# Performance work log

Measured on AMD Instinct MI355X. Metric: run time of the kernel, lower is better.

The kernel has to match this reference:

```python
import jax, jax.numpy as jnp
import numpy as np

N_NODES = 50000
N_EDGES = 1600000
NUM_GRAPHS = 512
IN_FEATS = 128
HIDDEN = 128
NUM_CLASSES = 10
STEPS = 3


def setup_inputs() -> dict:
    key = jax.random.key(0)
    ks = jax.random.split(key, 16)
    x = jax.random.normal(ks[0], (N_NODES, IN_FEATS), dtype=jnp.float32)
    edge_index = jax.random.randint(ks[1], (2, N_EDGES), 0, N_NODES, dtype=jnp.int64)
    batch = jnp.sort(jax.random.randint(ks[2], (N_NODES,), 0, NUM_GRAPHS, dtype=jnp.int64))
    s = 0.1
    W1 = jax.random.normal(ks[3], (IN_FEATS, HIDDEN), dtype=jnp.float32) * s
    b1 = jnp.zeros((HIDDEN,), dtype=jnp.float32)
    W2 = jax.random.normal(ks[4], (HIDDEN, HIDDEN), dtype=jnp.float32) * s
    b2 = jnp.zeros((HIDDEN,), dtype=jnp.float32)
    # LSTM: input 2*HIDDEN -> hidden HIDDEN, torch gate order i,f,g,o
    Wih = jax.random.normal(ks[5], (4 * HIDDEN, 2 * HIDDEN), dtype=jnp.float32) * s
    Whh = jax.random.normal(ks[6], (4 * HIDDEN, HIDDEN), dtype=jnp.float32) * s
    bih = jnp.zeros((4 * HIDDEN,), dtype=jnp.float32)
    bhh = jnp.zeros((4 * HIDDEN,), dtype=jnp.float32)
    Wl1 = jax.random.normal(ks[7], (2 * HIDDEN, HIDDEN), dtype=jnp.float32) * s
    bl1 = jnp.zeros((HIDDEN,), dtype=jnp.float32)
    Wl2 = jax.random.normal(ks[8], (HIDDEN, NUM_CLASSES), dtype=jnp.float32) * s
    bl2 = jnp.zeros((NUM_CLASSES,), dtype=jnp.float32)
    return dict(x=x, edge_index=edge_index, batch=batch, W1=W1, b1=b1, W2=W2, b2=b2,
                Wih=Wih, Whh=Whh, bih=bih, bhh=bhh, Wl1=Wl1, bl1=bl1, Wl2=Wl2, bl2=bl2)


def gcn_conv(x, src, dst, W, b, n_nodes):
    # PyG GCNConv: add self-loops, sym-normalized scatter-add aggregation
    loop = jnp.arange(n_nodes, dtype=src.dtype)
    s = jnp.concatenate([src, loop])
    d = jnp.concatenate([dst, loop])
    deg = jax.ops.segment_sum(jnp.ones_like(d, dtype=x.dtype), d, num_segments=n_nodes)
    dinv = jnp.where(deg > 0, jax.lax.rsqrt(jnp.maximum(deg, 1.0)), 0.0)
    norm = dinv[s] * dinv[d]  # [E+N]
    h = x @ W  # [N, out]
    agg = jax.ops.segment_sum(norm[:, None] * h[s], d, num_segments=n_nodes)
    return agg + b


def segment_softmax(e, seg, num_segments):
    m = jax.ops.segment_max(e, seg, num_segments=num_segments)
    m = jnp.where(jnp.isfinite(m), m, 0.0)
    z = jnp.exp(e - m[seg])
    denom = jax.ops.segment_sum(z, seg, num_segments=num_segments)
    return z / denom[seg]


def set2set(x, batch, Wih, Whh, bih, bhh, num_graphs, steps):
    D = x.shape[1]
    h = jnp.zeros((num_graphs, D), dtype=x.dtype)
    c = jnp.zeros((num_graphs, D), dtype=x.dtype)
    q_star = jnp.zeros((num_graphs, 2 * D), dtype=x.dtype)
    for _ in range(steps):
        gates = q_star @ Wih.T + h @ Whh.T + bih + bhh  # [B, 4D]
        i, f, g, o = jnp.split(gates, 4, axis=-1)
        c = jax.nn.sigmoid(f) * c + jax.nn.sigmoid(i) * jnp.tanh(g)
        h = jax.nn.sigmoid(o) * jnp.tanh(c)
        q = h
        e = jnp.sum(x * q[batch], axis=-1)  # [N]
        a = segment_softmax(e, batch, num_graphs)
        r = jax.ops.segment_sum(a[:, None] * x, batch, num_segments=num_graphs)  # [B, D]
        q_star = jnp.concatenate([q, r], axis=-1)
    return q_star


def reference(x, edge_index, batch, W1, b1, W2, b2, Wih, Whh, bih, bhh, Wl1, bl1, Wl2, bl2):
    n = x.shape[0]
    src, dst = edge_index[0], edge_index[1]
    h = jax.nn.relu(gcn_conv(x, src, dst, W1, b1, n))
    h = jax.nn.relu(gcn_conv(h, src, dst, W2, b2, n))
    out = set2set(h, batch, Wih, Whh, bih, bhh, NUM_GRAPHS, STEPS)  # [B, 2D]
    out = jax.nn.relu(out @ Wl1 + bl1)
    return out @ Wl2 + bl2
```

## Files before the change

kernel.cpp:

```cpp
#include <hip/hip_runtime.h>
#include <hip/hip_bf16.h>
#include <math.h>

#define N_NODES 50000
#define N_EDGES 1600000
#define NUM_GRAPHS 512
#define HIDDEN 128
#define NUM_CLASSES 10
#define STEPS 3

#define NB_SHIFT 6
#define NODES_PER_B (1 << NB_SHIFT)
#define NBUK ((N_NODES + NODES_PER_B - 1) / NODES_PER_B)
#define EPB 8192
#define NBLK ((N_EDGES + EPB - 1) / EPB)
#define MAXR 144
#define NCH 7

__device__ inline float bf2f(unsigned short h) {
    union { unsigned int u; float f; } v; v.u = ((unsigned int)h) << 16; return v.f;
}
__device__ inline unsigned short f2bf(float f) {
    union { float f; unsigned int u; } v; v.f = f;
    unsigned int r = (v.u + 0x7FFFu + ((v.u >> 16) & 1u)) >> 16;
    return (unsigned short)r;
}


__global__ void k_detect(const int* p, int* flag, int npairs) {
    int i = blockIdx.x * blockDim.x + threadIdx.x;
    if (i < npairs) {
        int v = p[2 * i + 1];
        if (v != 0) atomicOr(flag, 1);
    }
}

__global__ void k_goff(const void* batr, const int* flag, int* goff, int n, int ng) {
    int i = blockIdx.x * blockDim.x + threadIdx.x;
    if (i >= n) return;
    bool is32 = (*flag != 0);
    int b = is32 ? ((const int*)batr)[i] : (int)((const long long*)batr)[i];
    int prev = (i == 0) ? -1
             : (is32 ? ((const int*)batr)[i - 1] : (int)((const long long*)batr)[i - 1]);
    for (int g = prev + 1; g <= b; g++) goff[g] = i;
    if (i == n - 1) {
        for (int g = b + 1; g <= ng; g++) goff[g] = n;
    }
}

__global__ __launch_bounds__(256) void k_pack(const void* eidx, const int* flag,
                                              unsigned int* __restrict__ pdata,
                                              int* __restrict__ histg) {
    __shared__ int lh[NBUK];
    int b = blockIdx.x, t = threadIdx.x;
    for (int i = t; i < NBUK; i += 256) lh[i] = 0;
    __syncthreads();
    int base = b * EPB;
    int end = base + EPB; if (end > N_EDGES) end = N_EDGES;
    bool is32 = (*flag != 0);
    for (int i = base + t; i < end; i += 256) {
        int src, dst;
        if (is32) {
            const int* p = (const int*)eidx;
            src = p[i]; dst = p[N_EDGES + i];
        } else {
            const long long* p = (const long long*)eidx;
            src = (int)p[i]; dst = (int)p[N_EDGES + i];
        }
        pdata[i] = ((unsigned)src << 16) | (unsigned)dst;
        atomicAdd(&lh[dst >> NB_SHIFT], 1);
    }
    __syncthreads();
    for (int i = t; i < NBUK; i += 256) histg[(size_t)b * NBUK + i] = lh[i];
}

__global__ __launch_bounds__(256) void k_colscan(int* __restrict__ histg,
                                                 int* __restrict__ btot) {
    __shared__ int wsum[4];
    int k = blockIdx.x, t = threadIdx.x;
    int wid = t >> 6, lane = t & 63;
    int v = (t < NBLK) ? histg[(size_t)t * NBUK + k] : 0;
    int x = v;
#pragma unroll
    for (int o = 1; o < 64; o <<= 1) {
        int y = __shfl_up(x, o, 64);
        if (lane >= o) x += y;
    }
    if (lane == 63) wsum[wid] = x;
    __syncthreads();
    int add = 0;
    for (int w = 0; w < wid; w++) add += wsum[w];
    if (t < NBLK) histg[(size_t)t * NBUK + k] = add + x - v;
    if (t == NBLK - 1) btot[k] = add + x;
}

__global__ __launch_bounds__(1024) void k_scan(const int* cnt, int* offs, int n) {
    __shared__ int wsum[16];
    __shared__ int carry_sh;
    int t = threadIdx.x, wid = t >> 6, lane = t & 63;
    if (t == 0) { carry_sh = 0; offs[0] = 0; }
    __syncthreads();
    for (int base = 0; base < n; base += 1024) {
        int i = base + t;
        int v = (i < n) ? cnt[i] : 0;
        int x = v;
#pragma unroll
        for (int o = 1; o < 64; o <<= 1) {
            int y = __shfl_up(x, o, 64);
            if (lane >= o) x += y;
        }
        if (lane == 63) wsum[wid] = x;
        __syncthreads();
        if (wid == 0 && lane < 16) {
            int w = wsum[lane];
#pragma unroll
            for (int o = 1; o < 16; o <<= 1) {
                int y = __shfl_up(w, o, 16);
                if (lane >= o) w += y;
            }
            wsum[lane] = w;
        }
        __syncthreads();
        int add = carry_sh + (wid > 0 ? wsum[wid - 1] : 0);
        if (i < n) offs[i + 1] = add + x;
        __syncthreads();
        if (t == 0) carry_sh += wsum[15];
        __syncthreads();
    }
}

__global__ __launch_bounds__(256) void k_place(const unsigned int* __restrict__ pdata,
                                               const int* __restrict__ histg,
                                               const int* __restrict__ bbase,
                                               unsigned int* __restrict__ sdata) {
    __shared__ int lh[NBUK];
    __shared__ int lpre[NBUK];
    int b = blockIdx.x, t = threadIdx.x;
    for (int i = t; i < NBUK; i += 256) {
        lh[i] = 0;
        lpre[i] = bbase[i] + histg[(size_t)b * NBUK + i];
    }
    __syncthreads();
    int base = b * EPB;
    int end = base + EPB; if (end > N_EDGES) end = N_EDGES;
    for (int i = base + t; i < end; i += 256) {
        unsigned p = pdata[i];
        int k = (p & 0xFFFFu) >> NB_SHIFT;
        int pos = atomicAdd(&lh[k], 1);
        sdata[lpre[k] + pos] = p;
    }
}

__global__ __launch_bounds__(256) void k_build(const unsigned int* __restrict__ sdata,
                                               const int* __restrict__ bbase,
                                               const int* __restrict__ btot,
                                               float* __restrict__ dinv,
                                               int* __restrict__ offs,
                                               int* __restrict__ csr) {
    __shared__ int lc[NODES_PER_B][8];
    int b = blockIdx.x, t = threadIdx.x;
    for (int i = t; i < NODES_PER_B * 8; i += 256) ((int*)lc)[i] = 0;
    __syncthreads();
    int s0 = bbase[b], n = btot[b];
    const unsigned int* sd = sdata + s0;
    for (int e = t; e < n; e += 256) {
        unsigned p = sd[e];
        atomicAdd(&lc[p & (NODES_PER_B - 1)][(p >> 16) >> 13], 1);
    }
    __syncthreads();
    if (t < NODES_PER_B) {
        int cnts[NCH];
        int deg = 0;
#pragma unroll
        for (int c = 0; c < NCH; c++) { cnts[c] = lc[t][c]; deg += cnts[c]; }
        int x = deg;
#pragma unroll
        for (int o = 1; o < 64; o <<= 1) {
            int y = __shfl_up(x, o, 64);
            if (t >= o) x += y;
        }
        int nodestart = s0 + x - deg;
        int node = b * NODES_PER_B + t;
        if (node < N_NODES) {
            offs[node] = nodestart;
            dinv[node] = rsqrtf((float)(deg + 1));
        }
        int run = nodestart;
#pragma unroll
        for (int c = 0; c < NCH; c++) { lc[t][c] = run; run += cnts[c]; }
    }
    if (b == 0 && t == 255) offs[N_NODES] = N_EDGES;
    __syncthreads();
    for (int e = t; e < n; e += 256) {
        unsigned p = sd[e];
        int src = (int)(p >> 16);
        int pos = atomicAdd(&lc[p & (NODES_PER_B - 1)][src >> 13], 1);
        csr[pos] = src;
    }
}

__global__ __launch_bounds__(256) void k_gemm64(const float* __restrict__ X,
                                                const float* __restrict__ W,
                                                unsigned short* __restrict__ Hb,
                                                int nrows) {
    __shared__ float xs[64][128];
    int t = threadIdx.x;
    int a = t >> 5;
    int j4 = t & 31;
    int row0 = blockIdx.x * 64;
    for (int i = t; i < 64 * 32; i += 256) {
        int rr = i >> 5;
        int c4 = i & 31;
        int r = row0 + rr; if (r >= nrows) r = nrows - 1;
        ((float4*)xs[rr])[c4] = ((const float4*)X)[(size_t)r * 32 + c4];
    }
    __syncthreads();
    float4 acc[8];
#pragma unroll
    for (int i = 0; i < 8; i++) acc[i] = {0.f, 0.f, 0.f, 0.f};
    const float4* wp = (const float4*)W;
#pragma unroll 2
    for (int k0 = 0; k0 < 128; k0 += 4) {
        float4 w0 = wp[(k0 + 0) * 32 + j4];
        float4 w1 = wp[(k0 + 1) * 32 + j4];
        float4 w2 = wp[(k0 + 2) * 32 + j4];
        float4 w3 = wp[(k0 + 3) * 32 + j4];
#pragma unroll
        for (int i = 0; i < 8; i++) {
            float4 xv = *(const float4*)&xs[8 * a + i][k0];
            acc[i].x = fmaf(xv.x, w0.x, acc[i].x); acc[i].y = fmaf(xv.x, w0.y, acc[i].y);
            acc[i].z = fmaf(xv.x, w0.z, acc[i].z); acc[i].w = fmaf(xv.x, w0.w, acc[i].w);
            acc[i].x = fmaf(xv.y, w1.x, acc[i].x); acc[i].y = fmaf(xv.y, w1.y, acc[i].y);
            acc[i].z = fmaf(xv.y, w1.z, acc[i].z); acc[i].w = fmaf(xv.y, w1.w, acc[i].w);
            acc[i].x = fmaf(xv.z, w2.x, acc[i].x); acc[i].y = fmaf(xv.z, w2.y, acc[i].y);
            acc[i].z = fmaf(xv.z, w2.z, acc[i].z); acc[i].w = fmaf(xv.z, w2.w, acc[i].w);
            acc[i].x = fmaf(xv.w, w3.x, acc[i].x); acc[i].y = fmaf(xv.w, w3.y, acc[i].y);
            acc[i].z = fmaf(xv.w, w3.z, acc[i].z); acc[i].w = fmaf(xv.w, w3.w, acc[i].w);
        }
    }
#pragma unroll
    for (int i = 0; i < 8; i++) {
        int r = row0 + 8 * a + i;
        if (r < nrows) {
            ushort4 b4;
            b4.x = f2bf(acc[i].x); b4.y = f2bf(acc[i].y);
            b4.z = f2bf(acc[i].z); b4.w = f2bf(acc[i].w);
            ((ushort4*)Hb)[(size_t)r * 32 + j4] = b4;
        }
    }
}

__global__ __launch_bounds__(256) void k_agg(const unsigned short* __restrict__ Hb,
                                             const float* __restrict__ dinv,
                                             const int* __restrict__ offs,
                                             const int* __restrict__ csr,
                                             const float* __restrict__ b,
                                             float* __restrict__ out) {
    int wave = (blockIdx.x * blockDim.x + threadIdx.x) >> 6;
    int lane = threadIdx.x & 63;
    if (wave >= N_NODES) return;
    int n = wave;
    int half = lane >> 5;
    int l = lane & 31;
    float di = dinv[n];
    const ushort4* hbp = (const ushort4*)Hb;
    float4 acc = {0.f, 0.f, 0.f, 0.f};
    if (half == 0) {
        ushort4 hn = hbp[(size_t)n * 32 + l];
        acc.x = di * bf2f(hn.x); acc.y = di * bf2f(hn.y);
        acc.z = di * bf2f(hn.z); acc.w = di * bf2f(hn.w);
    }
    int e0 = offs[n], e1 = offs[n + 1];
    int j = e0 + half;
    for (; j + 14 < e1; j += 16) {
        int s[8]; float ds[8]; ushort4 a[8];
#pragma unroll
        for (int u = 0; u < 8; u++) s[u] = csr[j + 2 * u];
#pragma unroll
        for (int u = 0; u < 8; u++) ds[u] = dinv[s[u]];
#pragma unroll
        for (int u = 0; u < 8; u++) a[u] = hbp[(size_t)s[u] * 32 + l];
#pragma unroll
        for (int u = 0; u < 8; u++) {
            acc.x = fmaf(ds[u], bf2f(a[u].x), acc.x);
            acc.y = fmaf(ds[u], bf2f(a[u].y), acc.y);
            acc.z = fmaf(ds[u], bf2f(a[u].z), acc.z);
            acc.w = fmaf(ds[u], bf2f(a[u].w), acc.w);
        }
    }
    for (; j + 6 < e1; j += 8) {
        int s[4]; float ds[4]; ushort4 a[4];
#pragma unroll
        for (int u = 0; u < 4; u++) s[u] = csr[j + 2 * u];
#pragma unroll
        for (int u = 0; u < 4; u++) ds[u] = dinv[s[u]];
#pragma unroll
        for (int u = 0; u < 4; u++) a[u] = hbp[(size_t)s[u] * 32 + l];
#pragma unroll
        for (int u = 0; u < 4; u++) {
            acc.x = fmaf(ds[u], bf2f(a[u].x), acc.x);
            acc.y = fmaf(ds[u], bf2f(a[u].y), acc.y);
            acc.z = fmaf(ds[u], bf2f(a[u].z), acc.z);
            acc.w = fmaf(ds[u], bf2f(a[u].w), acc.w);
        }
    }
    for (; j < e1; j += 2) {
        int s = csr[j];
        float ds = dinv[s];
        ushort4 hs = hbp[(size_t)s * 32 + l];
        acc.x = fmaf(ds, bf2f(hs.x), acc.x); acc.y = fmaf(ds, bf2f(hs.y), acc.y);
        acc.z = fmaf(ds, bf2f(hs.z), acc.z); acc.w = fmaf(ds, bf2f(hs.w), acc.w);
    }
    acc.x += __shfl_xor(acc.x, 32, 64);
    acc.y += __shfl_xor(acc.y, 32, 64);
    acc.z += __shfl_xor(acc.z, 32, 64);
    acc.w += __shfl_xor(acc.w, 32, 64);
    if (half == 0) {
        const float4* bp = (const float4*)b;
        float4 bb = bp[l];
        float4 o4;
        o4.x = fmaxf(fmaf(di, acc.x, bb.x), 0.f);
        o4.y = fmaxf(fmaf(di, acc.y, bb.y), 0.f);
        o4.z = fmaxf(fmaf(di, acc.z, bb.z), 0.f);
        o4.w = fmaxf(fmaf(di, acc.w, bb.w), 0.f);
        ((float4*)out)[(size_t)n * 32 + l] = o4;
    }
}

__global__ __launch_bounds__(256) void k_gates(const float* __restrict__ qstar,
                                               const float* __restrict__ h,
                                               const float* __restrict__ Wih,
                                               const float* __restrict__ Whh,
                                               const float* __restrict__ bih,
                                               const float* __restrict__ bhh,
                                               float* __restrict__ gates) {
    __shared__ float As[64][33];
    __shared__ float Bs[64][33];
    int t = threadIdx.x;
    int tx = t & 15, ty = t >> 4;
    int gb = blockIdx.y * 64;
    int jb = blockIdx.x * 64;
    float acc[4][4];
#pragma unroll
    for (int i = 0; i < 4; i++)
#pragma unroll
        for (int j = 0; j < 4; j++) acc[i][j] = 0.f;
    for (int k0 = 0; k0 < 384; k0 += 32) {
        for (int i = t; i < 64 * 8; i += 256) {
            int r = i >> 3, c4 = i & 7;
            int k = k0 + c4 * 4;
            const float* srcA = (k < 256) ? (qstar + (size_t)(gb + r) * 256 + k)
                                          : (h + (size_t)(gb + r) * 128 + (k - 256));
            float4 va = *(const float4*)srcA;
            As[r][c4 * 4 + 0] = va.x; As[r][c4 * 4 + 1] = va.y;
            As[r][c4 * 4 + 2] = va.z; As[r][c4 * 4 + 3] = va.w;
            const float* srcB = (k < 256) ? (Wih + (size_t)(jb + r) * 256 + k)
                                          : (Whh + (size_t)(jb + r) * 128 + (k - 256));
            float4 vb = *(const float4*)srcB;
            Bs[r][c4 * 4 + 0] = vb.x; Bs[r][c4 * 4 + 1] = vb.y;
            Bs[r][c4 * 4 + 2] = vb.z; Bs[r][c4 * 4 + 3] = vb.w;
        }
        __syncthreads();
#pragma unroll 8
        for (int kk = 0; kk < 32; kk++) {
            float a[4], b[4];
#pragma unroll
            for (int i = 0; i < 4; i++) a[i] = As[ty * 4 + i][kk];
#pragma unroll
            for (int i = 0; i < 4; i++) b[i] = Bs[tx * 4 + i][kk];
#pragma unroll
            for (int i = 0; i < 4; i++)
#pragma unroll
                for (int j = 0; j < 4; j++) acc[i][j] = fmaf(a[i], b[j], acc[i][j]);
        }
        __syncthreads();
    }
#pragma unroll
    for (int j = 0; j < 4; j++) {
        int jj = jb + tx * 4 + j;
        float bias = bih[jj] + bhh[jj];
#pragma unroll
        for (int i = 0; i < 4; i++) {
            gates[(size_t)(gb + ty * 4 + i) * 512 + jj] = acc[i][j] + bias;
        }
    }
}

__global__ __launch_bounds__(256) void k_lstmel(const float* __restrict__ gates,
                                                const float* __restrict__ bih,
                                                const float* __restrict__ bhh,
                                                float* __restrict__ h,
                                                float* __restrict__ c,
                                                int first) {
    int i = blockIdx.x * 256 + threadIdx.x;
    if (i >= NUM_GRAPHS * 128) return;
    int b = i >> 7, d = i & 127;
    float iv, fv, gv, ov;
    if (first) {
        iv = bih[d] + bhh[d];
        fv = bih[128 + d] + bhh[128 + d];
        gv = bih[256 + d] + bhh[256 + d];
        ov = bih[384 + d] + bhh[384 + d];
    } else {
        const float* g = gates + (size_t)b * 512;
        iv = g[d]; fv = g[128 + d]; gv = g[256 + d]; ov = g[384 + d];
    }
    float si = 1.f / (1.f + expf(-iv));
    float sf = 1.f / (1.f + expf(-fv));
    float so = 1.f / (1.f + expf(-ov));
    float tg = tanhf(gv);
    float cold = first ? 0.f : c[i];
    float cn = sf * cold + si * tg;
    float hn = so * tanhf(cn);
    c[i] = cn;
    h[i] = hn;
}

__global__ __launch_bounds__(256) void k_attn(const float* __restrict__ X,
                                              const int* __restrict__ goff,
                                              const float* __restrict__ h,
                                              float* __restrict__ eg,
                                              float* __restrict__ qstar) {
    int b = blockIdx.x;
    int t = threadIdx.x;
    int wv = t >> 6, l = t & 63;
    int n0 = goff[b], n1 = goff[b + 1];
    int cnt = n1 - n0;
    __shared__ float rows[MAXR][128];
    __shared__ float q[128];
    __shared__ float ebuf[MAXR];
    __shared__ float red[256];
    __shared__ float wm[4];
    if (t < 128) q[t] = h[b * 128 + t];
    if (cnt <= MAXR) {
        for (int i = t; i < cnt * 32; i += 256) {
            int r = i >> 5, c4 = i & 31;
            ((float4*)rows[r])[c4] = ((const float4*)(X + (size_t)(n0 + r) * 128))[c4];
        }
        __syncthreads();
        const float2* qp = (const float2*)q;
        float2 q2 = qp[l];
        float mloc = -INFINITY;
        for (int n = wv; n < cnt; n += 4) {
            const float2* xp = (const float2*)rows[n];
            float2 x2 = xp[l];
            float p = x2.x * q2.x + x2.y * q2.y;
#pragma unroll
            for (int o = 32; o > 0; o >>= 1) p += __shfl_xor(p, o, 64);
            if (l == 0) ebuf[n] = p;
            mloc = fmaxf(mloc, p);
        }
        if (l == 0) wm[wv] = mloc;
        __syncthreads();
        float m = fmaxf(fmaxf(wm[0], wm[1]), fmaxf(wm[2], wm[3]));
        if (isinf(m)) m = 0.f;
        float s = 0.f;
        for (int n = t; n < cnt; n += 256) {
            float z = expf(ebuf[n] - m);
            ebuf[n] = z;
            s += z;
        }
        red[t] = s;
        __syncthreads();
        for (int o = 128; o > 0; o >>= 1) {
            if (t < o) red[t] += red[t + o];
            __syncthreads();
        }
        float denom = red[0];
        float inv = (denom > 0.f) ? 1.f / denom : 0.f;
        __syncthreads();
        int g = t >> 7, col = t & 127;
        float acc = 0.f;
        for (int n = g; n < cnt; n += 2) {
            acc = fmaf(ebuf[n] * inv, rows[n][col], acc);
        }
        red[t] = acc;
        __syncthreads();
        if (t < 128) {
            float r = red[t] + red[t + 128];
            qstar[b * 256 + t] = q[t];
            qstar[b * 256 + 128 + t] = r;
        }
    } else {
        __syncthreads();
        const float2* qp = (const float2*)q;
        float2 q2 = qp[l];
        float mloc = -INFINITY;
        for (int n = n0 + wv; n < n1; n += 4) {
            const float2* xp = (const float2*)(X + (size_t)n * 128);
            float2 x2 = xp[l];
            float p = x2.x * q2.x + x2.y * q2.y;
#pragma unroll
            for (int o = 32; o > 0; o >>= 1) p += __shfl_xor(p, o, 64);
            if (l == 0) eg[n] = p;
            mloc = fmaxf(mloc, p);
        }
        if (l == 0) wm[wv] = mloc;
        __syncthreads();
        float m = fmaxf(fmaxf(wm[0], wm[1]), fmaxf(wm[2], wm[3]));
        if (isinf(m)) m = 0.f;
        float s = 0.f;
        for (int n = n0 + t; n < n1; n += 256) {
            float z = expf(eg[n] - m);
            eg[n] = z;
            s += z;
        }
        red[t] = s;
        __syncthreads();
        for (int o = 128; o > 0; o >>= 1) {
            if (t < o) red[t] += red[t + o];
            __syncthreads();
        }
        float denom = red[0];
        float inv = (denom > 0.f) ? 1.f / denom : 0.f;
        __syncthreads();
        int g = t >> 7, col = t & 127;
        float acc = 0.f;
        for (int n = n0 + g; n < n1; n += 2) {
            acc = fmaf(eg[n] * inv, X[(size_t)n * 128 + col], acc);
        }
        red[t] = acc;
        __syncthreads();
        if (t < 128) {
            float r = red[t] + red[t + 128];
            qstar[b * 256 + t] = q[t];
            qstar[b * 256 + 128 + t] = r;
        }
    }
}

__global__ __launch_bounds__(128) void k_mlp(const float* __restrict__ qstar,
                                             const float* __restrict__ Wl1,
                                             const float* __restrict__ bl1,
                                             const float* __restrict__ Wl2,
                                             const float* __restrict__ bl2,
                                             float* __restrict__ out) {
    int b = blockIdx.x, t = threadIdx.x;
    __shared__ float qs[256];
    __shared__ float hid[128];
    qs[t] = qstar[b * 256 + t];
    qs[128 + t] = qstar[b * 256 + 128 + t];
    __syncthreads();
    float acc = bl1[t];
#pragma unroll 4
    for (int k = 0; k < 256; k++) acc = fmaf(qs[k], Wl1[k * 128 + t], acc);
    hid[t] = fmaxf(acc, 0.f);
    __syncthreads();
    if (t < NUM_CLASSES) {
        float o = bl2[t];
#pragma unroll 4
        for (int k = 0; k < 128; k++) o = fmaf(hid[k], Wl2[k * 10 + t], o);
        out[b * 10 + t] = o;
    }
}


extern "C" void kernel_launch(void* const* d_in, const int* in_sizes, int n_in,
                              void* d_out, int out_size, void* d_ws, size_t ws_size,
                              hipStream_t stream) {
    const float* x    = (const float*)d_in[0];
    const void*  eidx = d_in[1];
    const void*  batr = d_in[2];
    const float* W1   = (const float*)d_in[3];
    const float* b1   = (const float*)d_in[4];
    const float* W2   = (const float*)d_in[5];
    const float* b2   = (const float*)d_in[6];
    const float* Wih  = (const float*)d_in[7];
    const float* Whh  = (const float*)d_in[8];
    const float* bih  = (const float*)d_in[9];
    const float* bhh  = (const float*)d_in[10];
    const float* Wl1  = (const float*)d_in[11];
    const float* bl1  = (const float*)d_in[12];
    const float* Wl2  = (const float*)d_in[13];
    const float* bl2  = (const float*)d_in[14];
    float* out = (float*)d_out;

    char* ws = (char*)d_ws;
    size_t off = 0;
    auto alloc = [&](size_t bytes) {
        size_t r = off;
        off = (off + bytes + 255) & ~(size_t)255;
        return r;
    };
    float* A        = (float*)(ws + alloc((size_t)N_NODES * 128 * 4));
    int*   csr      = (int*)(ws + alloc((size_t)N_EDGES * 4));
    unsigned int* edgebuf = (unsigned int*)(ws + alloc((size_t)2 * N_EDGES * 4));
    int*   histg    = (int*)(ws + alloc((size_t)NBLK * NBUK * 4));
    int*   btot     = (int*)(ws + alloc((size_t)NBUK * 4));
    int*   bbase    = (int*)(ws + alloc((size_t)(NBUK + 1) * 4));
    int*   offs     = (int*)(ws + alloc((size_t)(N_NODES + 1) * 4));
    float* dinv     = (float*)(ws + alloc((size_t)N_NODES * 4));
    float* e        = (float*)(ws + alloc((size_t)N_NODES * 4));
    int*   goff     = (int*)(ws + alloc((size_t)(NUM_GRAPHS + 1) * 4));
    float* state    = (float*)(ws + alloc((size_t)(NUM_GRAPHS * 128 * 2 + NUM_GRAPHS * 256) * 4));
    float* gates    = (float*)(ws + alloc((size_t)NUM_GRAPHS * 512 * 4));
    int*   flag     = (int*)(ws + alloc(4));
    if (off > ws_size) return;

    unsigned int* pdata = edgebuf;
    unsigned int* sdata = edgebuf + N_EDGES;
    unsigned short* Hb = (unsigned short*)edgebuf;

    float* h_lstm = state;
    float* c_lstm = state + NUM_GRAPHS * 128;
    float* qstar  = state + NUM_GRAPHS * 256;

    const int B = 256;
    hipMemsetAsync(flag, 0, 4, stream);
    k_detect<<<(4096 + B - 1) / B, B, 0, stream>>>((const int*)eidx, flag, 4096);
    k_goff<<<(N_NODES + B - 1) / B, B, 0, stream>>>(batr, flag, goff, N_NODES, NUM_GRAPHS);
    k_pack<<<NBLK, 256, 0, stream>>>(eidx, flag, pdata, histg);
    k_colscan<<<NBUK, 256, 0, stream>>>(histg, btot);
    k_scan<<<1, 1024, 0, stream>>>(btot, bbase, NBUK);
    k_place<<<NBLK, 256, 0, stream>>>(pdata, histg, bbase, sdata);
    k_build<<<NBUK, 256, 0, stream>>>(sdata, bbase, btot, dinv, offs, csr);
    k_gemm64<<<(N_NODES + 63) / 64, 256, 0, stream>>>(x, W1, Hb, N_NODES);
    k_agg<<<(N_NODES + 3) / 4, 256, 0, stream>>>(Hb, dinv, offs, csr, b1, A);
    k_gemm64<<<(N_NODES + 63) / 64, 256, 0, stream>>>(A, W2, Hb, N_NODES);
    k_agg<<<(N_NODES + 3) / 4, 256, 0, stream>>>(Hb, dinv, offs, csr, b2, A);
    for (int s = 0; s < STEPS; s++) {
        if (s > 0) {
            dim3 gg(8, 8);
            k_gates<<<gg, 256, 0, stream>>>(qstar, h_lstm, Wih, Whh, bih, bhh, gates);
        }
        k_lstmel<<<NUM_GRAPHS * 128 / 256, 256, 0, stream>>>(gates, bih, bhh, h_lstm, c_lstm, s == 0);
        k_attn<<<NUM_GRAPHS, 256, 0, stream>>>(A, goff, h_lstm, e, qstar);
    }
    k_mlp<<<NUM_GRAPHS, 128, 0, stream>>>(qstar, Wl1, bl1, Wl2, bl2, out);
}
```

Baseline: 394.7 us.

## Use split-bf16 MFMA for node GEMMs and fuse LSTM cell into attention

Replaces the FP32 FMA node-feature GEMM with a matrix-core kernel that splits activations and weights into high and low bf16 parts and issues three bf16 MFMAs per tile, keeping near-fp32 accuracy. Weights are pre-transposed and split by a small conversion kernel, then staged into XOR-swizzled shared memory. Separately, the LSTM elementwise cell update is folded into the attention kernel, removing one launch per step. The cost is extra conversion launches and three MFMAs per tile, plus uncoalesced 2-byte output stores.

Measured after the change: 361.8 us. 8.3% less time.

```diff
diff --git a/kernel.cpp b/kernel.cpp
--- a/kernel.cpp
+++ b/kernel.cpp
@@ -16,6 +16,9 @@
 #define NBLK ((N_EDGES + EPB - 1) / EPB)
 #define MAXR 144
 #define NCH 7
+
+typedef __attribute__((ext_vector_type(8))) short bf16x8;
+typedef __attribute__((ext_vector_type(4))) float f32x4;
 
 __device__ inline float bf2f(unsigned short h) {
     union { unsigned int u; float f; } v; v.u = ((unsigned int)h) << 16; return v.f;
@@ -199,53 +202,76 @@
     }
 }
 
-__global__ __launch_bounds__(256) void k_gemm64(const float* __restrict__ X,
-                                                const float* __restrict__ W,
-                                                unsigned short* __restrict__ Hb,
-                                                int nrows) {
-    __shared__ float xs[64][128];
+__global__ void k_cvtw(const float* __restrict__ W,
+                       unsigned short* __restrict__ Wth,
+                       unsigned short* __restrict__ Wtl) {
+    int i = blockIdx.x * 256 + threadIdx.x;
+    if (i >= 128 * 128) return;
+    int k = i >> 7, j = i & 127;
+    float w = W[i];
+    unsigned short h = f2bf(w);
+    float lo = w - bf2f(h);
+    Wth[j * 128 + k] = h;
+    Wtl[j * 128 + k] = f2bf(lo);
+}
+
+__global__ __launch_bounds__(256) void k_gemm_mfma(const float* __restrict__ X,
+                                                   const unsigned short* __restrict__ Wth,
+                                                   const unsigned short* __restrict__ Wtl,
+                                                   unsigned short* __restrict__ Hb,
+                                                   int nrows) {
+    __shared__ bf16x8 wh[2048];
+    __shared__ bf16x8 wl[2048];
     int t = threadIdx.x;
-    int a = t >> 5;
-    int j4 = t & 31;
-    int row0 = blockIdx.x * 64;
-    for (int i = t; i < 64 * 32; i += 256) {
-        int rr = i >> 5;
-        int c4 = i & 31;
-        int r = row0 + rr; if (r >= nrows) r = nrows - 1;
-        ((float4*)xs[rr])[c4] = ((const float4*)X)[(size_t)r * 32 + c4];
-    }
-    __syncthreads();
-    float4 acc[8];
-#pragma unroll
-    for (int i = 0; i < 8; i++) acc[i] = {0.f, 0.f, 0.f, 0.f};
-    const float4* wp = (const float4*)W;
-#pragma unroll 2
-    for (int k0 = 0; k0 < 128; k0 += 4) {
-        float4 w0 = wp[(k0 + 0) * 32 + j4];
-        float4 w1 = wp[(k0 + 1) * 32 + j4];
-        float4 w2 = wp[(k0 + 2) * 32 + j4];
-        float4 w3 = wp[(k0 + 3) * 32 + j4];
+    for (int i = t; i < 2048; i += 256) {
+        int n = i >> 4;
+        int slot = i ^ (n & 7);
+        wh[slot] = ((const bf16x8*)Wth)[i];
+        wl[slot] = ((const bf16x8*)Wtl)[i];
+    }
+    __syncthreads();
+    int w = t >> 6, l = t & 63;
+    int lrow = l & 15, lk = l >> 4;
+    int arow = blockIdx.x * 64 + w * 16 + lrow;
+    int rr = (arow < nrows) ? arow : nrows - 1;
+    const float* xrow = X + (size_t)rr * 128;
+    f32x4 acc[8];
+#pragma unroll
+    for (int nt = 0; nt < 8; nt++) acc[nt] = (f32x4){0.f, 0.f, 0.f, 0.f};
+#pragma unroll
+    for (int kk = 0; kk < 4; kk++) {
+        int k = kk * 32 + lk * 8;
+        float4 x0 = *(const float4*)(xrow + k);
+        float4 x1 = *(const float4*)(xrow + k + 4);
+        float xv[8] = {x0.x, x0.y, x0.z, x0.w, x1.x, x1.y, x1.z, x1.w};
+        union { bf16x8 v; unsigned short s[8]; } ah, al;
 #pragma unroll
         for (int i = 0; i < 8; i++) {
-            float4 xv = *(const float4*)&xs[8 * a + i][k0];
-            acc[i].x = fmaf(xv.x, w0.x, acc[i].x); acc[i].y = fmaf(xv.x, w0.y, acc[i].y);
-            acc[i].z = fmaf(xv.x, w0.z, acc[i].z); acc[i].w = fmaf(xv.x, w0.w, acc[i].w);
-            acc[i].x = fmaf(xv.y, w1.x, acc[i].x); acc[i].y = fmaf(xv.y, w1.y, acc[i].y);
-            acc[i].z = fmaf(xv.y, w1.z, acc[i].z); acc[i].w = fmaf(xv.y, w1.w, acc[i].w);
-            acc[i].x = fmaf(xv.z, w2.x, acc[i].x); acc[i].y = fmaf(xv.z, w2.y, acc[i].y);
-            acc[i].z = fmaf(xv.z, w2.z, acc[i].z); acc[i].w = fmaf(xv.z, w2.w, acc[i].w);
-            acc[i].x = fmaf(xv.w, w3.x, acc[i].x); acc[i].y = fmaf(xv.w, w3.y, acc[i].y);
-            acc[i].z = fmaf(xv.w, w3.z, acc[i].z); acc[i].w = fmaf(xv.w, w3.w, acc[i].w);
-        }
-    }
-#pragma unroll
-    for (int i = 0; i < 8; i++) {
-        int r = row0 + 8 * a + i;
-        if (r < nrows) {
-            ushort4 b4;
-            b4.x = f2bf(acc[i].x); b4.y = f2bf(acc[i].y);
-            b4.z = f2bf(acc[i].z); b4.w = f2bf(acc[i].w);
-            ((ushort4*)Hb)[(size_t)r * 32 + j4] = b4;
+            unsigned u = __float_as_uint(xv[i]);
+            unsigned short hi = (unsigned short)(u >> 16);
+            ah.s[i] = hi;
+            float lo = xv[i] - __uint_as_float((unsigned)hi << 16);
+            al.s[i] = (unsigned short)(__float_as_uint(lo) >> 16);
+        }
+#pragma unroll
+        for (int nt = 0; nt < 8; nt++) {
+            int n = nt * 16 + lrow;
+            int slot = (n * 16 + kk * 4 + lk) ^ (n & 7);
+            bf16x8 bh = wh[slot];
+            bf16x8 bl = wl[slot];
+            acc[nt] = __builtin_amdgcn_mfma_f32_16x16x32_bf16(ah.v, bh, acc[nt], 0, 0, 0);
+            acc[nt] = __builtin_amdgcn_mfma_f32_16x16x32_bf16(ah.v, bl, acc[nt], 0, 0, 0);
+            acc[nt] = __builtin_amdgcn_mfma_f32_16x16x32_bf16(al.v, bh, acc[nt], 0, 0, 0);
+        }
+    }
+    int obase = blockIdx.x * 64 + w * 16 + lk * 4;
+#pragma unroll
+    for (int r = 0; r < 4; r++) {
+        int orow = obase + r;
+        if (orow < nrows) {
+            unsigned short* dst = Hb + (size_t)orow * 128 + lrow;
+#pragma unroll
+            for (int nt = 0; nt < 8; nt++) dst[nt * 16] = f2bf(acc[nt][r]);
         }
     }
 }
@@ -386,41 +412,16 @@
     }
 }
 
-__global__ __launch_bounds__(256) void k_lstmel(const float* __restrict__ gates,
-                                                const float* __restrict__ bih,
-                                                const float* __restrict__ bhh,
-                                                float* __restrict__ h,
-                                                float* __restrict__ c,
-                                                int first) {
-    int i = blockIdx.x * 256 + threadIdx.x;
-    if (i >= NUM_GRAPHS * 128) return;
-    int b = i >> 7, d = i & 127;
-    float iv, fv, gv, ov;
-    if (first) {
-        iv = bih[d] + bhh[d];
-        fv = bih[128 + d] + bhh[128 + d];
-        gv = bih[256 + d] + bhh[256 + d];
-        ov = bih[384 + d] + bhh[384 + d];
-    } else {
-        const float* g = gates + (size_t)b * 512;
-        iv = g[d]; fv = g[128 + d]; gv = g[256 + d]; ov = g[384 + d];
-    }
-    float si = 1.f / (1.f + expf(-iv));
-    float sf = 1.f / (1.f + expf(-fv));
-    float so = 1.f / (1.f + expf(-ov));
-    float tg = tanhf(gv);
-    float cold = first ? 0.f : c[i];
-    float cn = sf * cold + si * tg;
-    float hn = so * tanhf(cn);
-    c[i] = cn;
-    h[i] = hn;
-}
-
 __global__ __launch_bounds__(256) void k_attn(const float* __restrict__ X,
                                               const int* __restrict__ goff,
-                                              const float* __restrict__ h,
+                                              const float* __restrict__ gates,
+                                              const float* __restrict__ bih,
+                                              const float* __restrict__ bhh,
+                                              float* __restrict__ h,
+                                              float* __restrict__ c,
                                               float* __restrict__ eg,
-                                              float* __restrict__ qstar) {
+                                              float* __restrict__ qstar,
+                                              int first) {
     int b = blockIdx.x;
     int t = threadIdx.x;
     int wv = t >> 6, l = t & 63;
@@ -431,7 +432,28 @@
     __shared__ float ebuf[MAXR];
     __shared__ float red[256];
     __shared__ float wm[4];
-    if (t < 128) q[t] = h[b * 128 + t];
+    if (t < 128) {
+        float iv, fv, gv, ov;
+        if (first) {
+            iv = bih[t] + bhh[t];
+            fv = bih[128 + t] + bhh[128 + t];
+            gv = bih[256 + t] + bhh[256 + t];
+            ov = bih[384 + t] + bhh[384 + t];
+        } else {
+            const float* g = gates + (size_t)b * 512;
+            iv = g[t]; fv = g[128 + t]; gv = g[256 + t]; ov = g[384 + t];
+        }
+        float si = 1.f / (1.f + expf(-iv));
+        float sf = 1.f / (1.f + expf(-fv));
+        float so = 1.f / (1.f + expf(-ov));
+        float tg = tanhf(gv);
+        float cold = first ? 0.f : c[b * 128 + t];
+        float cn = sf * cold + si * tg;
+        float hn = so * tanhf(cn);
+        c[b * 128 + t] = cn;
+        h[b * 128 + t] = hn;
+        q[t] = hn;
+    }
     if (cnt <= MAXR) {
         for (int i = t; i < cnt * 32; i += 256) {
             int r = i >> 5, c4 = i & 31;
@@ -594,6 +616,10 @@
     int*   goff     = (int*)(ws + alloc((size_t)(NUM_GRAPHS + 1) * 4));
     float* state    = (float*)(ws + alloc((size_t)(NUM_GRAPHS * 128 * 2 + NUM_GRAPHS * 256) * 4));
     float* gates    = (float*)(ws + alloc((size_t)NUM_GRAPHS * 512 * 4));
+    unsigned short* Wth1 = (unsigned short*)(ws + alloc((size_t)128 * 128 * 2));
+    unsigned short* Wtl1 = (unsigned short*)(ws + alloc((size_t)128 * 128 * 2));
+    unsigned short* Wth2 = (unsigned short*)(ws + alloc((size_t)128 * 128 * 2));
+    unsigned short* Wtl2 = (unsigned short*)(ws + alloc((size_t)128 * 128 * 2));
     int*   flag     = (int*)(ws + alloc(4));
     if (off > ws_size) return;
 
@@ -614,17 +640,19 @@
     k_scan<<<1, 1024, 0, stream>>>(btot, bbase, NBUK);
     k_place<<<NBLK, 256, 0, stream>>>(pdata, histg, bbase, sdata);
     k_build<<<NBUK, 256, 0, stream>>>(sdata, bbase, btot, dinv, offs, csr);
-    k_gemm64<<<(N_NODES + 63) / 64, 256, 0, stream>>>(x, W1, Hb, N_NODES);
+    k_cvtw<<<64, 256, 0, stream>>>(W1, Wth1, Wtl1);
+    k_cvtw<<<64, 256, 0, stream>>>(W2, Wth2, Wtl2);
+    k_gemm_mfma<<<(N_NODES + 63) / 64, 256, 0, stream>>>(x, Wth1, Wtl1, Hb, N_NODES);
     k_agg<<<(N_NODES + 3) / 4, 256, 0, stream>>>(Hb, dinv, offs, csr, b1, A);
-    k_gemm64<<<(N_NODES + 63) / 64, 256, 0, stream>>>(A, W2, Hb, N_NODES);
+    k_gemm_mfma<<<(N_NODES + 63) / 64, 256, 0, stream>>>(A, Wth2, Wtl2, Hb, N_NODES);
     k_agg<<<(N_NODES + 3) / 4, 256, 0, stream>>>(Hb, dinv, offs, csr, b2, A);
     for (int s = 0; s < STEPS; s++) {
         if (s > 0) {
             dim3 gg(8, 8);
             k_gates<<<gg, 256, 0, stream>>>(qstar, h_lstm, Wih, Whh, bih, bhh, gates);
         }
-        k_lstmel<<<NUM_GRAPHS * 128 / 256, 256, 0, stream>>>(gates, bih, bhh, h_lstm, c_lstm, s == 0);
-        k_attn<<<NUM_GRAPHS, 256, 0, stream>>>(A, goff, h_lstm, e, qstar);
+        k_attn<<<NUM_GRAPHS, 256, 0, stream>>>(A, goff, gates, bih, bhh,
+                                               h_lstm, c_lstm, e, qstar, s == 0);
     }
     k_mlp<<<NUM_GRAPHS, 128, 0, stream>>>(qstar, Wl1, bl1, Wl2, bl2, out);
 }
```
